# Kernel tuning notes

Measured on AMD Instinct MI355X. Metric: run time of the kernel, lower is better.

The kernel has to match this reference:

```python
import jax, jax.numpy as jnp
import numpy as np

VOCAB = 32000; DIM = 512; NL = 6; B = 2; L = 1024
DI = 2 * DIM      # d_inner (expand=2)
DS = 16           # d_state
DC = 4            # d_conv
DR = DIM // 16    # dt_rank = ceil(512/16) = 32


def setup_inputs() -> dict:
    key = jax.random.key(0)
    ks = jax.random.split(key, 10)
    s = 0.02
    tokens = jax.random.randint(ks[0], (B, L), 0, VOCAB)
    pos_emb = jax.random.normal(ks[1], (1, L, DIM)) * s
    embed = jax.random.normal(ks[2], (VOCAB, DIM)) * s
    lm_w = jax.random.normal(ks[3], (VOCAB, DIM)) * s
    lm_b = jnp.zeros((VOCAB,), jnp.float32)
    in_proj_w = jax.random.normal(ks[4], (NL, 2 * DI, DIM)) * s
    conv_w = jax.random.normal(ks[5], (NL, DI, DC)) * s
    conv_b = jnp.zeros((NL, DI), jnp.float32)
    x_proj_w = jax.random.normal(ks[6], (NL, DR + 2 * DS, DI)) * s
    dt_proj_w = jax.random.normal(ks[7], (NL, DI, DR)) * s
    dt_proj_b = jnp.broadcast_to(jnp.log(jnp.expm1(jnp.float32(0.01))), (NL, DI)).astype(jnp.float32)
    A_log = jnp.log(jnp.broadcast_to(jnp.arange(1, DS + 1, dtype=jnp.float32), (NL, DI, DS)))
    Dp = jnp.ones((NL, DI), jnp.float32)
    out_w = jax.random.normal(ks[8], (NL, DIM, DI)) * s
    ln_g = jnp.ones((NL, DIM), jnp.float32)
    ln_b = jnp.zeros((NL, DIM), jnp.float32)
    return dict(tokens=tokens, pos_emb=pos_emb, embed=embed, lm_w=lm_w, lm_b=lm_b,
                in_proj_w=in_proj_w, conv_w=conv_w, conv_b=conv_b, x_proj_w=x_proj_w,
                dt_proj_w=dt_proj_w, dt_proj_b=dt_proj_b, A_log=A_log, Dp=Dp,
                out_w=out_w, ln_g=ln_g, ln_b=ln_b)


def silu(x):
    return x * jax.nn.sigmoid(x)


def layernorm(x, g, b, eps=1e-5):
    mu = jnp.mean(x, -1, keepdims=True)
    var = jnp.var(x, -1, keepdims=True)
    return (x - mu) * jax.lax.rsqrt(var + eps) * g + b


def causal_dwconv(x, w, b):
    # x: (B,L,DI), w: (DI,DC) depthwise, left-pad causal
    xp = jnp.pad(x, ((0, 0), (DC - 1, 0), (0, 0)))
    y = b
    for k in range(DC):
        y = y + w[:, k] * xp[:, k:k + x.shape[1], :]
    return y


def selective_scan(u, dt, A, Bm, Cm, Dp):
    # u,dt: (B,L,DI); A: (DI,DS); Bm,Cm: (B,L,DS)
    dA = jnp.exp(dt[..., None] * A)                       # (B,L,DI,DS)
    dBu = dt[..., None] * Bm[:, :, None, :] * u[..., None]
    h0 = jnp.zeros((u.shape[0], DI, DS), u.dtype)

    def step(h, inp):
        dA_t, dBu_t, C_t = inp
        h = dA_t * h + dBu_t
        y = jnp.einsum('bdn,bn->bd', h, C_t)
        return h, y

    _, ys = jax.lax.scan(step, h0, (dA.transpose(1, 0, 2, 3),
                                    dBu.transpose(1, 0, 2, 3),
                                    Cm.transpose(1, 0, 2)))
    return ys.transpose(1, 0, 2) + u * Dp


def mamba_block(x, in_w, cw, cb, xp_w, dtw, dtb, A_log, Dp, ow):
    xz = jnp.einsum('bld,ed->ble', x, in_w)               # (B,L,2*DI)
    xc, z = jnp.split(xz, 2, axis=-1)
    xc = silu(causal_dwconv(xc, cw, cb))
    x_dbl = jnp.einsum('bld,ed->ble', xc, xp_w)           # (B,L,DR+2*DS)
    dt, Bm, Cm = jnp.split(x_dbl, [DR, DR + DS], axis=-1)
    dt = jax.nn.softplus(jnp.einsum('blr,dr->bld', dt, dtw) + dtb)
    A = -jnp.exp(A_log)
    y = selective_scan(xc, dt, A, Bm, Cm, Dp)
    y = y * silu(z)
    return jnp.einsum('bld,ed->ble', y, ow)


def reference(tokens, pos_emb, embed, lm_w, lm_b, in_proj_w, conv_w, conv_b,
              x_proj_w, dt_proj_w, dt_proj_b, A_log, Dp, out_w, ln_g, ln_b):
    x = embed[tokens] + pos_emb[:, :tokens.shape[1]]
    for i in range(NL):
        res = x
        x = mamba_block(x, in_proj_w[i], conv_w[i], conv_b[i], x_proj_w[i],
                        dt_proj_w[i], dt_proj_b[i], A_log[i], Dp[i], out_w[i])
        x = layernorm(x + res, ln_g[i], ln_b[i])
    return jnp.einsum('bld,vd->blv', x, lm_w) + lm_b
```

## Files before the change

kernel.cpp:

```cpp
#include <hip/hip_runtime.h>
#include <hip/hip_bf16.h>
#include <math.h>

#define BB 2
#define LL 1024
#define DIM 512
#define NL 6
#define DI 1024
#define DS 16
#define DC 4
#define DR 32
#define VOCAB 32000
#define M_ROWS (BB * LL)
#define CCH 64
#define CHLEN (LL / CCH)
#define KSPLIT 8

typedef unsigned short u16;
typedef __attribute__((ext_vector_type(8))) short bf16x8;
typedef __attribute__((ext_vector_type(4))) float f32x4;

__device__ __forceinline__ u16 f2bf(float f) {
    unsigned u = __float_as_uint(f);
    u += 0x7FFF + ((u >> 16) & 1);
    return (u16)(u >> 16);
}
#define SWZ(r, c) ((c) ^ (((r) >> 1) & 3))

__global__ __launch_bounds__(256) void cast_bf16(const float* __restrict__ in,
                                                 u16* __restrict__ out, int n8) {
    int idx = blockIdx.x * 256 + threadIdx.x;
    if (idx >= n8) return;
    float4 v0 = ((const float4*)in)[idx * 2];
    float4 v1 = ((const float4*)in)[idx * 2 + 1];
    union { u16 h[8]; int4 v; } r;
    r.h[0] = f2bf(v0.x); r.h[1] = f2bf(v0.y); r.h[2] = f2bf(v0.z); r.h[3] = f2bf(v0.w);
    r.h[4] = f2bf(v1.x); r.h[5] = f2bf(v1.y); r.h[6] = f2bf(v1.z); r.h[7] = f2bf(v1.w);
    ((int4*)out)[idx] = r.v;
}

__global__ __launch_bounds__(256) void embed_kernel(const int* __restrict__ tok,
                                                    const float* __restrict__ pos,
                                                    const float* __restrict__ emb,
                                                    float* __restrict__ x,
                                                    u16* __restrict__ xb) {
    int idx = blockIdx.x * 256 + threadIdx.x;
    int d = idx & (DIM - 1);
    int l = (idx >> 9) & (LL - 1);
    int b = idx >> 19;
    int t = tok[b * LL + l];
    float v = emb[(size_t)t * DIM + d] + pos[l * DIM + d];
    x[idx] = v;
    xb[idx] = f2bf(v);
}

__global__ __launch_bounds__(256) void gemm_bf16(const u16* __restrict__ A,
                                                 const u16* __restrict__ W,
                                                 const float* __restrict__ bias,
                                                 float* __restrict__ C,
                                                 int M, int N, int K,
                                                 int lda, int ldw, int mode) {
    __shared__ __align__(16) u16 As[3 * 4096];
    __shared__ __align__(16) u16 Ws[3 * 4096];
    const int t = threadIdx.x;
    const int l = t & 63;
    const int w = t >> 6;
    const int nwg = gridDim.x;
    const int q = nwg >> 3, r8 = nwg & 7;
    const int xcd = blockIdx.x & 7, rank = blockIdx.x >> 3;
    const int wgid = (xcd < r8 ? xcd * (q + 1) : r8 * (q + 1) + (xcd - r8) * q) + rank;
    const int Mb = M >> 7;
    const int bm = (wgid % Mb) * 128;
    const int bn = (wgid / Mb) * 128;
    const int wm = (w >> 1) * 64;
    const int wn = (w & 1) * 64;

    f32x4 acc[4][4] = {};
    const int nt = K >> 5;

    auto STAGE = [&](int bufi, int k0) {
#pragma unroll
        for (int p = 0; p < 2; ++p) {
            const int i = (p * 4 + w) * 64 + l;
            const int row = i >> 2;
            const int kq = SWZ(row, i & 3);
            __builtin_amdgcn_global_load_lds(
                (const __attribute__((address_space(1))) unsigned int*)
                    (A + (size_t)(bm + row) * lda + k0 + kq * 8),
                (__attribute__((address_space(3))) unsigned int*)
                    (As + bufi * 4096 + (p * 4 + w) * 512),
                16, 0, 0);
            __builtin_amdgcn_global_load_lds(
                (const __attribute__((address_space(1))) unsigned int*)
                    (W + (size_t)(bn + row) * ldw + k0 + kq * 8),
                (__attribute__((address_space(3))) unsigned int*)
                    (Ws + bufi * 4096 + (p * 4 + w) * 512),
                16, 0, 0);
        }
    };
    auto COMPUTE = [&](int bufi) {
        const u16* Ab = As + bufi * 4096;
        const u16* Wb = Ws + bufi * 4096;
#pragma unroll
        for (int mi = 0; mi < 4; ++mi) {
            const int ar = wm + mi * 16 + (l & 15);
            bf16x8 a = *(const bf16x8*)(Ab + ar * 32 + SWZ(ar, l >> 4) * 8);
#pragma unroll
            for (int ni = 0; ni < 4; ++ni) {
                const int wr = wn + ni * 16 + (l & 15);
                bf16x8 b = *(const bf16x8*)(Wb + wr * 32 + SWZ(wr, l >> 4) * 8);
                acc[mi][ni] = __builtin_amdgcn_mfma_f32_16x16x32_bf16(b, a, acc[mi][ni], 0, 0, 0);
            }
        }
    };

    STAGE(0, 0);
    if (nt == 1) {
        asm volatile("s_waitcnt vmcnt(0)\ns_barrier" ::: "memory");
        COMPUTE(0);
    } else {
        STAGE(1, 32);
        int b0 = 0;
        for (int tt = 0; tt < nt - 2; ++tt) {
            int b2 = b0 + 2; if (b2 >= 3) b2 -= 3;
            STAGE(b2, (tt + 2) << 5);
            asm volatile("s_waitcnt vmcnt(8)\ns_barrier" ::: "memory");
            COMPUTE(b0);
            asm volatile("s_waitcnt lgkmcnt(0)\ns_barrier" ::: "memory");
            ++b0; if (b0 == 3) b0 = 0;
        }
        asm volatile("s_waitcnt vmcnt(4)\ns_barrier" ::: "memory");
        COMPUTE(b0);
        asm volatile("s_waitcnt lgkmcnt(0)\ns_barrier" ::: "memory");
        ++b0; if (b0 == 3) b0 = 0;
        asm volatile("s_waitcnt vmcnt(0)\ns_barrier" ::: "memory");
        COMPUTE(b0);
    }

#pragma unroll
    for (int mi = 0; mi < 4; ++mi) {
        const int row = bm + wm + mi * 16 + (l & 15);
#pragma unroll
        for (int ni = 0; ni < 4; ++ni) {
            const int col = bn + wn + ni * 16 + ((l >> 4) << 2);
            float4 v;
            v.x = acc[mi][ni][0]; v.y = acc[mi][ni][1];
            v.z = acc[mi][ni][2]; v.w = acc[mi][ni][3];
            if (bias != nullptr) {
                float4 b4 = *(const float4*)(bias + col);
                v.x += b4.x; v.y += b4.y; v.z += b4.z; v.w += b4.w;
            }
            if (mode == 1) {
                v.x = (v.x > 20.f) ? v.x : log1pf(__expf(v.x));
                v.y = (v.y > 20.f) ? v.y : log1pf(__expf(v.y));
                v.z = (v.z > 20.f) ? v.z : log1pf(__expf(v.z));
                v.w = (v.w > 20.f) ? v.w : log1pf(__expf(v.w));
            }
            *(float4*)(C + (size_t)row * N + col) = v;
        }
    }
}

__global__ __launch_bounds__(256) void gemm_n64(const u16* __restrict__ A,
                                                const u16* __restrict__ W,
                                                float* __restrict__ out,
                                                int lda, int ldw, int ldc,
                                                int KS, int pstride) {
    __shared__ __align__(16) u16 As[3 * 4096];
    __shared__ __align__(16) u16 Ws[3 * 2048];
    const int t = threadIdx.x;
    const int l = t & 63;
    const int w = t >> 6;
    const int kz = blockIdx.x;
    const int bm = blockIdx.y * 128;
    const int bnn = blockIdx.z * 64;
    const int wm = w * 32;

    f32x4 acc[2][4] = {};
    const int nt = KS >> 5;
    const int kbeg = kz * KS;

    auto STAGE = [&](int bufi, int k0) {
#pragma unroll
        for (int p = 0; p < 2; ++p) {
            const int i = p * 256 + w * 64 + l;
            const int row = i >> 2;
            const int kq = SWZ(row, i & 3);
            __builtin_amdgcn_global_load_lds(
                (const __attribute__((address_space(1))) unsigned int*)
                    (A + (size_t)(bm + row) * lda + k0 + kq * 8),
                (__attribute__((address_space(3))) unsigned int*)
                    (As + bufi * 4096 + (p * 256 + w * 64) * 8),
                16, 0, 0);
        }
        {
            const int i = w * 64 + l;
            const int row = i >> 2;
            const int kq = SWZ(row, i & 3);
            __builtin_amdgcn_global_load_lds(
                (const __attribute__((address_space(1))) unsigned int*)
                    (W + (size_t)(bnn + row) * ldw + k0 + kq * 8),
                (__attribute__((address_space(3))) unsigned int*)
                    (Ws + bufi * 2048 + (w * 64) * 8),
                16, 0, 0);
        }
    };
    auto COMPUTE = [&](int bufi) {
        const u16* Ab = As + bufi * 4096;
        const u16* Wb = Ws + bufi * 2048;
#pragma unroll
        for (int mi = 0; mi < 2; ++mi) {
            const int ar = wm + mi * 16 + (l & 15);
            bf16x8 a = *(const bf16x8*)(Ab + ar * 32 + SWZ(ar, l >> 4) * 8);
#pragma unroll
            for (int ni = 0; ni < 4; ++ni) {
                const int wr = ni * 16 + (l & 15);
                bf16x8 b = *(const bf16x8*)(Wb + wr * 32 + SWZ(wr, l >> 4) * 8);
                acc[mi][ni] = __builtin_amdgcn_mfma_f32_16x16x32_bf16(b, a, acc[mi][ni], 0, 0, 0);
            }
        }
    };

    STAGE(0, kbeg);
    if (nt == 1) {
        asm volatile("s_waitcnt vmcnt(0)\ns_barrier" ::: "memory");
        COMPUTE(0);
    } else {
        STAGE(1, kbeg + 32);
        int b0 = 0;
        for (int tt = 0; tt < nt - 2; ++tt) {
            int b2 = b0 + 2; if (b2 >= 3) b2 -= 3;
            STAGE(b2, kbeg + ((tt + 2) << 5));
            asm volatile("s_waitcnt vmcnt(6)\ns_barrier" ::: "memory");
            COMPUTE(b0);
            asm volatile("s_waitcnt lgkmcnt(0)\ns_barrier" ::: "memory");
            ++b0; if (b0 == 3) b0 = 0;
        }
        asm volatile("s_waitcnt vmcnt(3)\ns_barrier" ::: "memory");
        COMPUTE(b0);
        asm volatile("s_waitcnt lgkmcnt(0)\ns_barrier" ::: "memory");
        ++b0; if (b0 == 3) b0 = 0;
        asm volatile("s_waitcnt vmcnt(0)\ns_barrier" ::: "memory");
        COMPUTE(b0);
    }

    float* op = out + (size_t)kz * pstride;
#pragma unroll
    for (int mi = 0; mi < 2; ++mi) {
        const int row = bm + wm + mi * 16 + (l & 15);
#pragma unroll
        for (int ni = 0; ni < 4; ++ni) {
            const int col = bnn + ni * 16 + ((l >> 4) << 2);
            float4 v;
            v.x = acc[mi][ni][0]; v.y = acc[mi][ni][1];
            v.z = acc[mi][ni][2]; v.w = acc[mi][ni][3];
            *(float4*)(op + (size_t)row * ldc + col) = v;
        }
    }
}

__global__ __launch_bounds__(256) void xdreduce(const float* __restrict__ Pf,
                                                float* __restrict__ xd,
                                                u16* __restrict__ xdb) {
    int idx = blockIdx.x * 256 + threadIdx.x;
    float s = 0.f;
#pragma unroll
    for (int kz = 0; kz < KSPLIT; ++kz)
        s += Pf[(size_t)kz * (M_ROWS * 64) + idx];
    xd[idx] = s;
    xdb[idx] = f2bf(s);
}

__global__ __launch_bounds__(256) void conv_silu(const float* __restrict__ xz,
                                                 const float* __restrict__ cw,
                                                 const float* __restrict__ cb,
                                                 float* __restrict__ xc,
                                                 u16* __restrict__ xcb) {
    int idx = blockIdx.x * 256 + threadIdx.x;
    int c = idx & (DI - 1);
    int l = (idx >> 10) & (LL - 1);
    int b = idx >> 20;
    float acc = cb[c];
#pragma unroll
    for (int k = 0; k < DC; ++k) {
        int ll = l + k - (DC - 1);
        if (ll >= 0)
            acc += cw[c * DC + k] * xz[((size_t)(b * LL + ll)) * (2 * DI) + c];
    }
    float v = acc / (1.f + __expf(-acc));
    xc[idx] = v;
    xcb[idx] = f2bf(v);
}

__global__ __launch_bounds__(256) void scan_pass1(const float* __restrict__ xc,
                                                  const float* __restrict__ dt,
                                                  const float* __restrict__ xdbl,
                                                  const float* __restrict__ A_log,
                                                  float* __restrict__ S,
                                                  float* __restrict__ Q) {
    const int d = blockIdx.x * 256 + threadIdx.x;
    const int b = blockIdx.y;
    const int c = blockIdx.z;
    float a[DS];
#pragma unroll
    for (int q = 0; q < 4; ++q) {
        float4 al = *(const float4*)(A_log + d * DS + q * 4);
        a[q * 4 + 0] = -__expf(al.x);
        a[q * 4 + 1] = -__expf(al.y);
        a[q * 4 + 2] = -__expf(al.z);
        a[q * 4 + 3] = -__expf(al.w);
    }
    float Qr[DS];
#pragma unroll
    for (int n = 0; n < DS; ++n) Qr[n] = 0.f;
    float Ssum = 0.f;

    const int l0 = c * CHLEN;
    const float* dtp = dt + ((size_t)b * LL + l0) * DI + d;
    const float* up  = xc + ((size_t)b * LL + l0) * DI + d;
    const float* xdp = xdbl + ((size_t)b * LL + l0) * 64 + DR;

    for (int l = 0; l < CHLEN; ++l) {
        float dtv = dtp[(size_t)l * DI];
        float uv  = up[(size_t)l * DI];
        float wv = dtv * uv;
        Ssum += dtv;
#pragma unroll
        for (int q = 0; q < 4; ++q) {
            float4 Bv = *(const float4*)(xdp + l * 64 + q * 4);
            float dA0 = __expf(dtv * a[q * 4 + 0]);
            float dA1 = __expf(dtv * a[q * 4 + 1]);
            float dA2 = __expf(dtv * a[q * 4 + 2]);
            float dA3 = __expf(dtv * a[q * 4 + 3]);
            Qr[q * 4 + 0] = dA0 * Qr[q * 4 + 0] + wv * Bv.x;
            Qr[q * 4 + 1] = dA1 * Qr[q * 4 + 1] + wv * Bv.y;
            Qr[q * 4 + 2] = dA2 * Qr[q * 4 + 2] + wv * Bv.z;
            Qr[q * 4 + 3] = dA3 * Qr[q * 4 + 3] + wv * Bv.w;
        }
    }
    S[((size_t)b * CCH + c) * DI + d] = Ssum;
    float* Qp = Q + (((size_t)b * CCH + c) * DI + d) * DS;
#pragma unroll
    for (int q = 0; q < 4; ++q) {
        float4 o;
        o.x = Qr[q * 4 + 0]; o.y = Qr[q * 4 + 1];
        o.z = Qr[q * 4 + 2]; o.w = Qr[q * 4 + 3];
        *(float4*)(Qp + q * 4) = o;
    }
}

__global__ __launch_bounds__(256) void scan_pass2(const float* __restrict__ A_log,
                                                  const float* __restrict__ S,
                                                  float* __restrict__ Q) {
    const int idx = blockIdx.x * 256 + threadIdx.x;
    const int b = idx >> 14;
    const int dn = idx & 16383;
    const int d = dn >> 4;
    const float a = -__expf(A_log[dn]);
    float h = 0.f;
    for (int c = 0; c < CCH; ++c) {
        const size_t soff = ((size_t)b * CCH + c) * DI + d;
        const size_t qoff = ((size_t)b * CCH + c) * (size_t)(DI * DS) + dn;
        float P = __expf(a * S[soff]);
        float qv = Q[qoff];
        Q[qoff] = h;
        h = P * h + qv;
    }
}

__global__ __launch_bounds__(256) void scan_pass3(const float* __restrict__ xc,
                                                  const float* __restrict__ dt,
                                                  const float* __restrict__ xdbl,
                                                  const float* __restrict__ xz,
                                                  const float* __restrict__ A_log,
                                                  const float* __restrict__ Dpp,
                                                  const float* __restrict__ Q,
                                                  u16* __restrict__ y) {
    const int d = blockIdx.x * 256 + threadIdx.x;
    const int b = blockIdx.y;
    const int c = blockIdx.z;
    float a[DS];
#pragma unroll
    for (int q = 0; q < 4; ++q) {
        float4 al = *(const float4*)(A_log + d * DS + q * 4);
        a[q * 4 + 0] = -__expf(al.x);
        a[q * 4 + 1] = -__expf(al.y);
        a[q * 4 + 2] = -__expf(al.z);
        a[q * 4 + 3] = -__expf(al.w);
    }
    float h[DS];
    const float* Qp = Q + (((size_t)b * CCH + c) * DI + d) * DS;
#pragma unroll
    for (int q = 0; q < 4; ++q) {
        float4 hv = *(const float4*)(Qp + q * 4);
        h[q * 4 + 0] = hv.x; h[q * 4 + 1] = hv.y;
        h[q * 4 + 2] = hv.z; h[q * 4 + 3] = hv.w;
    }
    const float dp = Dpp[d];

    const int l0 = c * CHLEN;
    const float* dtp = dt + ((size_t)b * LL + l0) * DI + d;
    const float* up  = xc + ((size_t)b * LL + l0) * DI + d;
    const float* xdp = xdbl + ((size_t)b * LL + l0) * 64 + DR;
    const float* zp  = xz + ((size_t)b * LL + l0) * (2 * DI) + DI + d;
    u16* yp = y + ((size_t)b * LL + l0) * DI + d;

    for (int l = 0; l < CHLEN; ++l) {
        float dtv = dtp[(size_t)l * DI];
        float uv  = up[(size_t)l * DI];
        float wv = dtv * uv;
        float p = 0.f;
#pragma unroll
        for (int q = 0; q < 4; ++q) {
            float4 Bv = *(const float4*)(xdp + l * 64 + q * 4);
            float4 Cv = *(const float4*)(xdp + l * 64 + 16 + q * 4);
            float dA0 = __expf(dtv * a[q * 4 + 0]);
            float dA1 = __expf(dtv * a[q * 4 + 1]);
            float dA2 = __expf(dtv * a[q * 4 + 2]);
            float dA3 = __expf(dtv * a[q * 4 + 3]);
            h[q * 4 + 0] = dA0 * h[q * 4 + 0] + wv * Bv.x;
            h[q * 4 + 1] = dA1 * h[q * 4 + 1] + wv * Bv.y;
            h[q * 4 + 2] = dA2 * h[q * 4 + 2] + wv * Bv.z;
            h[q * 4 + 3] = dA3 * h[q * 4 + 3] + wv * Bv.w;
            p += h[q * 4 + 0] * Cv.x + h[q * 4 + 1] * Cv.y +
                 h[q * 4 + 2] * Cv.z + h[q * 4 + 3] * Cv.w;
        }
        float zv = zp[(size_t)l * (2 * DI)];
        float g = zv / (1.f + __expf(-zv));
        yp[(size_t)l * DI] = f2bf((p + uv * dp) * g);
    }
}

__global__ __launch_bounds__(256) void add_ln(const float* __restrict__ o,
                                              float* __restrict__ x,
                                              const float* __restrict__ g,
                                              const float* __restrict__ b,
                                              u16* __restrict__ xb) {
    int m = blockIdx.x;
    int t = threadIdx.x;
    const float* xr = x + (size_t)m * DIM;
    const float* orr = o + (size_t)m * DIM;
    float v0 = xr[t] + orr[t];
    float v1 = xr[t + 256] + orr[t + 256];
    float s = v0 + v1;
    float ss = v0 * v0 + v1 * v1;
#pragma unroll
    for (int off = 32; off > 0; off >>= 1) {
        s += __shfl_down(s, off, 64);
        ss += __shfl_down(ss, off, 64);
    }
    __shared__ float sb[4], ssb[4];
    int w = t >> 6;
    if ((t & 63) == 0) { sb[w] = s; ssb[w] = ss; }
    __syncthreads();
    float stot = sb[0] + sb[1] + sb[2] + sb[3];
    float sstot = ssb[0] + ssb[1] + ssb[2] + ssb[3];
    float mean = stot * (1.f / DIM);
    float var = sstot * (1.f / DIM) - mean * mean;
    float rs = rsqrtf(var + 1e-5f);
    float* xw = x + (size_t)m * DIM;
    float o0 = (v0 - mean) * rs * g[t] + b[t];
    float o1 = (v1 - mean) * rs * g[t + 256] + b[t + 256];
    xw[t] = o0;
    xw[t + 256] = o1;
    xb[(size_t)m * DIM + t] = f2bf(o0);
    xb[(size_t)m * DIM + t + 256] = f2bf(o1);
}

extern "C" void kernel_launch(void* const* d_in, const int* in_sizes, int n_in,
                              void* d_out, int out_size, void* d_ws, size_t ws_size,
                              hipStream_t stream) {
    const int*   tokens = (const int*)d_in[0];
    const float* pos    = (const float*)d_in[1];
    const float* emb    = (const float*)d_in[2];
    const float* lm_w   = (const float*)d_in[3];
    const float* lm_b   = (const float*)d_in[4];
    const float* in_w   = (const float*)d_in[5];
    const float* cw     = (const float*)d_in[6];
    const float* cb     = (const float*)d_in[7];
    const float* xpw    = (const float*)d_in[8];
    const float* dtw    = (const float*)d_in[9];
    const float* dtb    = (const float*)d_in[10];
    const float* A_log  = (const float*)d_in[11];
    const float* Dpp    = (const float*)d_in[12];
    const float* ow     = (const float*)d_in[13];
    const float* lng    = (const float*)d_in[14];
    const float* lnb    = (const float*)d_in[15];
    float* out = (float*)d_out;

    float* ws = (float*)d_ws;
    float* x    = ws;
    float* xz   = x + 1048576;
    float* xc   = xz + 4194304;
    float* xd   = xc + 2097152;
    float* dt   = xd + 131072;
    float* o    = dt + 2097152;
    float* S    = o + 1048576;
    float* Qb   = S + 131072;
    float* Pf   = Qb + 2097152;
    u16* xb     = (u16*)(Pf + 1048576);
    u16* yb     = xb + 1048576;
    u16* xcb    = yb + 2097152;
    u16* xdb    = xcb + 2097152;
    u16* lm_wb  = xdb + 131072;
    u16* in_wb  = lm_wb + 16384000;
    u16* owb    = in_wb + 6291456;
    u16* xpwb   = owb + 3145728;
    u16* dtwb   = xpwb + 393216;

    cast_bf16<<<16384000 / 8 / 256, 256, 0, stream>>>(lm_w, lm_wb, 16384000 / 8);
    cast_bf16<<<6291456 / 8 / 256, 256, 0, stream>>>(in_w, in_wb, 6291456 / 8);
    cast_bf16<<<3145728 / 8 / 256, 256, 0, stream>>>(ow, owb, 3145728 / 8);
    cast_bf16<<<393216 / 8 / 256, 256, 0, stream>>>(xpw, xpwb, 393216 / 8);
    cast_bf16<<<196608 / 8 / 256, 256, 0, stream>>>(dtw, dtwb, 196608 / 8);

    embed_kernel<<<M_ROWS * DIM / 256, 256, 0, stream>>>(tokens, pos, emb, x, xb);

    for (int i = 0; i < NL; ++i) {
        gemm_bf16<<<(2048 / 128) * (M_ROWS / 128), 256, 0, stream>>>(
            xb, in_wb + (size_t)i * 2048 * 512, nullptr, xz,
            M_ROWS, 2048, 512, 512, 512, 0);
        conv_silu<<<M_ROWS * DI / 256, 256, 0, stream>>>(
            xz, cw + (size_t)i * DI * DC, cb + (size_t)i * DI, xc, xcb);
        gemm_n64<<<dim3(KSPLIT, M_ROWS / 128, 1), 256, 0, stream>>>(
            xcb, xpwb + (size_t)i * 64 * 1024, Pf,
            1024, 1024, 64, 1024 / KSPLIT, M_ROWS * 64);
        xdreduce<<<M_ROWS * 64 / 256, 256, 0, stream>>>(Pf, xd, xdb);
        gemm_bf16<<<(1024 / 128) * (M_ROWS / 128), 256, 0, stream>>>(
            xdb, dtwb + (size_t)i * 1024 * 32, dtb + (size_t)i * DI, dt,
            M_ROWS, 1024, 32, 64, 32, 1);
        scan_pass1<<<dim3(DI / 256, BB, CCH), 256, 0, stream>>>(
            xc, dt, xd, A_log + (size_t)i * DI * DS, S, Qb);
        scan_pass2<<<(BB * DI * DS) / 256, 256, 0, stream>>>(
            A_log + (size_t)i * DI * DS, S, Qb);
        scan_pass3<<<dim3(DI / 256, BB, CCH), 256, 0, stream>>>(
            xc, dt, xd, xz, A_log + (size_t)i * DI * DS, Dpp + (size_t)i * DI, Qb, yb);
        gemm_n64<<<dim3(1, M_ROWS / 128, 512 / 64), 256, 0, stream>>>(
            yb, owb + (size_t)i * 512 * 1024, o,
            1024, 1024, 512, 1024, 0);
        add_ln<<<M_ROWS, 256, 0, stream>>>(
            o, x, lng + (size_t)i * DIM, lnb + (size_t)i * DIM, xb);
    }

    gemm_bf16<<<(VOCAB / 128) * (M_ROWS / 128), 256, 0, stream>>>(
        xb, lm_wb, lm_b, out, M_ROWS, VOCAB, 512, 512, 512, 0);
}
```

Before: 908.3 us.

## Fuse xd reduction with fp32 dt projection, merge weight casts, double-buffer GEMMs

```diff
diff --git a/kernel.cpp b/kernel.cpp
--- a/kernel.cpp
+++ b/kernel.cpp
@@ -27,16 +27,26 @@
 }
 #define SWZ(r, c) ((c) ^ (((r) >> 1) & 3))
 
-__global__ __launch_bounds__(256) void cast_bf16(const float* __restrict__ in,
-                                                 u16* __restrict__ out, int n8) {
+__global__ __launch_bounds__(256) void cast_all(const float* __restrict__ lm,
+                                                const float* __restrict__ inw,
+                                                const float* __restrict__ ow,
+                                                const float* __restrict__ xp,
+                                                u16* __restrict__ lmb,
+                                                u16* __restrict__ inb,
+                                                u16* __restrict__ owb_,
+                                                u16* __restrict__ xpb) {
     int idx = blockIdx.x * 256 + threadIdx.x;
-    if (idx >= n8) return;
-    float4 v0 = ((const float4*)in)[idx * 2];
-    float4 v1 = ((const float4*)in)[idx * 2 + 1];
+    const float* src; u16* dst; int off;
+    if (idx < 2048000)      { src = lm;  dst = lmb;  off = idx; }
+    else if (idx < 2834432) { src = inw; dst = inb;  off = idx - 2048000; }
+    else if (idx < 3227648) { src = ow;  dst = owb_; off = idx - 2834432; }
+    else                    { src = xp;  dst = xpb;  off = idx - 3227648; }
+    float4 v0 = ((const float4*)src)[off * 2];
+    float4 v1 = ((const float4*)src)[off * 2 + 1];
     union { u16 h[8]; int4 v; } r;
     r.h[0] = f2bf(v0.x); r.h[1] = f2bf(v0.y); r.h[2] = f2bf(v0.z); r.h[3] = f2bf(v0.w);
     r.h[4] = f2bf(v1.x); r.h[5] = f2bf(v1.y); r.h[6] = f2bf(v1.z); r.h[7] = f2bf(v1.w);
-    ((int4*)out)[idx] = r.v;
+    ((int4*)dst)[off] = r.v;
 }
 
 __global__ __launch_bounds__(256) void embed_kernel(const int* __restrict__ tok,
@@ -59,9 +69,9 @@
                                                  const float* __restrict__ bias,
                                                  float* __restrict__ C,
                                                  int M, int N, int K,
-                                                 int lda, int ldw, int mode) {
-    __shared__ __align__(16) u16 As[3 * 4096];
-    __shared__ __align__(16) u16 Ws[3 * 4096];
+                                                 int lda, int ldw) {
+    __shared__ __align__(16) u16 As[2 * 4096];
+    __shared__ __align__(16) u16 Ws[2 * 4096];
     const int t = threadIdx.x;
     const int l = t & 63;
     const int w = t >> 6;
@@ -115,26 +125,15 @@
     };
 
     STAGE(0, 0);
-    if (nt == 1) {
-        asm volatile("s_waitcnt vmcnt(0)\ns_barrier" ::: "memory");
-        COMPUTE(0);
-    } else {
-        STAGE(1, 32);
-        int b0 = 0;
-        for (int tt = 0; tt < nt - 2; ++tt) {
-            int b2 = b0 + 2; if (b2 >= 3) b2 -= 3;
-            STAGE(b2, (tt + 2) << 5);
-            asm volatile("s_waitcnt vmcnt(8)\ns_barrier" ::: "memory");
-            COMPUTE(b0);
-            asm volatile("s_waitcnt lgkmcnt(0)\ns_barrier" ::: "memory");
-            ++b0; if (b0 == 3) b0 = 0;
-        }
-        asm volatile("s_waitcnt vmcnt(4)\ns_barrier" ::: "memory");
-        COMPUTE(b0);
+    for (int tt = 0; tt < nt; ++tt) {
+        if (tt + 1 < nt) {
+            STAGE((tt + 1) & 1, (tt + 1) << 5);
+            asm volatile("s_waitcnt vmcnt(4)\ns_barrier" ::: "memory");
+        } else {
+            asm volatile("s_waitcnt vmcnt(0)\ns_barrier" ::: "memory");
+        }
+        COMPUTE(tt & 1);
         asm volatile("s_waitcnt lgkmcnt(0)\ns_barrier" ::: "memory");
-        ++b0; if (b0 == 3) b0 = 0;
-        asm volatile("s_waitcnt vmcnt(0)\ns_barrier" ::: "memory");
-        COMPUTE(b0);
     }
 
 #pragma unroll
@@ -150,12 +149,6 @@
                 float4 b4 = *(const float4*)(bias + col);
                 v.x += b4.x; v.y += b4.y; v.z += b4.z; v.w += b4.w;
             }
-            if (mode == 1) {
-                v.x = (v.x > 20.f) ? v.x : log1pf(__expf(v.x));
-                v.y = (v.y > 20.f) ? v.y : log1pf(__expf(v.y));
-                v.z = (v.z > 20.f) ? v.z : log1pf(__expf(v.z));
-                v.w = (v.w > 20.f) ? v.w : log1pf(__expf(v.w));
-            }
             *(float4*)(C + (size_t)row * N + col) = v;
         }
     }
@@ -166,8 +159,8 @@
                                                 float* __restrict__ out,
                                                 int lda, int ldw, int ldc,
                                                 int KS, int pstride) {
-    __shared__ __align__(16) u16 As[3 * 4096];
-    __shared__ __align__(16) u16 Ws[3 * 2048];
+    __shared__ __align__(16) u16 As[2 * 4096];
+    __shared__ __align__(16) u16 Ws[2 * 2048];
     const int t = threadIdx.x;
     const int l = t & 63;
     const int w = t >> 6;
@@ -222,26 +215,15 @@
     };
 
     STAGE(0, kbeg);
-    if (nt == 1) {
-        asm volatile("s_waitcnt vmcnt(0)\ns_barrier" ::: "memory");
-        COMPUTE(0);
-    } else {
-        STAGE(1, kbeg + 32);
-        int b0 = 0;
-        for (int tt = 0; tt < nt - 2; ++tt) {
-            int b2 = b0 + 2; if (b2 >= 3) b2 -= 3;
-            STAGE(b2, kbeg + ((tt + 2) << 5));
-            asm volatile("s_waitcnt vmcnt(6)\ns_barrier" ::: "memory");
-            COMPUTE(b0);
-            asm volatile("s_waitcnt lgkmcnt(0)\ns_barrier" ::: "memory");
-            ++b0; if (b0 == 3) b0 = 0;
-        }
-        asm volatile("s_waitcnt vmcnt(3)\ns_barrier" ::: "memory");
-        COMPUTE(b0);
+    for (int tt = 0; tt < nt; ++tt) {
+        if (tt + 1 < nt) {
+            STAGE((tt + 1) & 1, kbeg + ((tt + 1) << 5));
+            asm volatile("s_waitcnt vmcnt(3)\ns_barrier" ::: "memory");
+        } else {
+            asm volatile("s_waitcnt vmcnt(0)\ns_barrier" ::: "memory");
+        }
+        COMPUTE(tt & 1);
         asm volatile("s_waitcnt lgkmcnt(0)\ns_barrier" ::: "memory");
-        ++b0; if (b0 == 3) b0 = 0;
-        asm volatile("s_waitcnt vmcnt(0)\ns_barrier" ::: "memory");
-        COMPUTE(b0);
     }
 
     float* op = out + (size_t)kz * pstride;
@@ -259,16 +241,59 @@
     }
 }
 
-__global__ __launch_bounds__(256) void xdreduce(const float* __restrict__ Pf,
+__global__ __launch_bounds__(256) void xdred_dt(const float* __restrict__ Pf,
+                                                const float* __restrict__ dtw,
+                                                const float* __restrict__ dtb,
                                                 float* __restrict__ xd,
-                                                u16* __restrict__ xdb) {
-    int idx = blockIdx.x * 256 + threadIdx.x;
-    float s = 0.f;
-#pragma unroll
-    for (int kz = 0; kz < KSPLIT; ++kz)
-        s += Pf[(size_t)kz * (M_ROWS * 64) + idx];
-    xd[idx] = s;
-    xdb[idx] = f2bf(s);
+                                                float* __restrict__ dt) {
+    __shared__ float xds[16][64];
+    const int m0 = blockIdx.x * 16;
+    const int t = threadIdx.x;
+    for (int i = t; i < 1024; i += 256) {
+        int r = i >> 6, c = i & 63;
+        float s = 0.f;
+#pragma unroll
+        for (int kz = 0; kz < KSPLIT; ++kz)
+            s += Pf[(size_t)kz * (M_ROWS * 64) + (m0 + r) * 64 + c];
+        xds[r][c] = s;
+        xd[(m0 + r) * 64 + c] = s;
+    }
+    __syncthreads();
+    const int d0 = t * 4;
+    float acc[16][4];
+#pragma unroll
+    for (int r = 0; r < 16; ++r)
+#pragma unroll
+        for (int j = 0; j < 4; ++j) acc[r][j] = 0.f;
+#pragma unroll
+    for (int qk = 0; qk < 8; ++qk) {
+        float4 w0 = *(const float4*)(dtw + (d0 + 0) * DR + qk * 4);
+        float4 w1 = *(const float4*)(dtw + (d0 + 1) * DR + qk * 4);
+        float4 w2 = *(const float4*)(dtw + (d0 + 2) * DR + qk * 4);
+        float4 w3 = *(const float4*)(dtw + (d0 + 3) * DR + qk * 4);
+#pragma unroll
+        for (int r = 0; r < 16; ++r) {
+            float4 xv = *(const float4*)&xds[r][qk * 4];
+            acc[r][0] += w0.x * xv.x + w0.y * xv.y + w0.z * xv.z + w0.w * xv.w;
+            acc[r][1] += w1.x * xv.x + w1.y * xv.y + w1.z * xv.z + w1.w * xv.w;
+            acc[r][2] += w2.x * xv.x + w2.y * xv.y + w2.z * xv.z + w2.w * xv.w;
+            acc[r][3] += w3.x * xv.x + w3.y * xv.y + w3.z * xv.z + w3.w * xv.w;
+        }
+    }
+    float4 bv = *(const float4*)(dtb + d0);
+#pragma unroll
+    for (int r = 0; r < 16; ++r) {
+        float4 v;
+        v.x = acc[r][0] + bv.x;
+        v.y = acc[r][1] + bv.y;
+        v.z = acc[r][2] + bv.z;
+        v.w = acc[r][3] + bv.w;
+        v.x = (v.x > 20.f) ? v.x : log1pf(__expf(v.x));
+        v.y = (v.y > 20.f) ? v.y : log1pf(__expf(v.y));
+        v.z = (v.z > 20.f) ? v.z : log1pf(__expf(v.z));
+        v.w = (v.w > 20.f) ? v.w : log1pf(__expf(v.w));
+        *(float4*)(dt + (size_t)(m0 + r) * DI + d0) = v;
+    }
 }
 
 __global__ __launch_bounds__(256) void conv_silu(const float* __restrict__ xz,
@@ -501,34 +526,27 @@
     u16* xb     = (u16*)(Pf + 1048576);
     u16* yb     = xb + 1048576;
     u16* xcb    = yb + 2097152;
-    u16* xdb    = xcb + 2097152;
-    u16* lm_wb  = xdb + 131072;
+    u16* lm_wb  = xcb + 2097152;
     u16* in_wb  = lm_wb + 16384000;
     u16* owb    = in_wb + 6291456;
     u16* xpwb   = owb + 3145728;
-    u16* dtwb   = xpwb + 393216;
-
-    cast_bf16<<<16384000 / 8 / 256, 256, 0, stream>>>(lm_w, lm_wb, 16384000 / 8);
-    cast_bf16<<<6291456 / 8 / 256, 256, 0, stream>>>(in_w, in_wb, 6291456 / 8);
-    cast_bf16<<<3145728 / 8 / 256, 256, 0, stream>>>(ow, owb, 3145728 / 8);
-    cast_bf16<<<393216 / 8 / 256, 256, 0, stream>>>(xpw, xpwb, 393216 / 8);
-    cast_bf16<<<196608 / 8 / 256, 256, 0, stream>>>(dtw, dtwb, 196608 / 8);
+
+    cast_all<<<12800, 256, 0, stream>>>(lm_w, in_w, ow, xpw,
+                                        lm_wb, in_wb, owb, xpwb);
 
     embed_kernel<<<M_ROWS * DIM / 256, 256, 0, stream>>>(tokens, pos, emb, x, xb);
 
     for (int i = 0; i < NL; ++i) {
         gemm_bf16<<<(2048 / 128) * (M_ROWS / 128), 256, 0, stream>>>(
             xb, in_wb + (size_t)i * 2048 * 512, nullptr, xz,
-            M_ROWS, 2048, 512, 512, 512, 0);
+            M_ROWS, 2048, 512, 512, 512);
         conv_silu<<<M_ROWS * DI / 256, 256, 0, stream>>>(
             xz, cw + (size_t)i * DI * DC, cb + (size_t)i * DI, xc, xcb);
         gemm_n64<<<dim3(KSPLIT, M_ROWS / 128, 1), 256, 0, stream>>>(
             xcb, xpwb + (size_t)i * 64 * 1024, Pf,
             1024, 1024, 64, 1024 / KSPLIT, M_ROWS * 64);
-        xdreduce<<<M_ROWS * 64 / 256, 256, 0, stream>>>(Pf, xd, xdb);
-        gemm_bf16<<<(1024 / 128) * (M_ROWS / 128), 256, 0, stream>>>(
-            xdb, dtwb + (size_t)i * 1024 * 32, dtb + (size_t)i * DI, dt,
-            M_ROWS, 1024, 32, 64, 32, 1);
+        xdred_dt<<<128, 256, 0, stream>>>(
+            Pf, dtw + (size_t)i * DI * DR, dtb + (size_t)i * DI, xd, dt);
         scan_pass1<<<dim3(DI / 256, BB, CCH), 256, 0, stream>>>(
             xc, dt, xd, A_log + (size_t)i * DI * DS, S, Qb);
         scan_pass2<<<(BB * DI * DS) / 256, 256, 0, stream>>>(
@@ -543,5 +561,5 @@
     }
 
     gemm_bf16<<<(VOCAB / 128) * (M_ROWS / 128), 256, 0, stream>>>(
-        xb, lm_wb, lm_b, out, M_ROWS, VOCAB, 512, 512, 512, 0);
-}
+        xb, lm_wb, lm_b, out, M_ROWS, VOCAB, 512, 512, 512);
+}
```

Result: slower. 1.522 ms (+67.5%).
